# Kernel optimization log

Hardware: AMD Instinct MI355X
Metric: run time of the kernel (lower is better)

The kernel has to match this reference:

```python
import jax, jax.numpy as jnp
import numpy as np


def _roi_crop_resize(fm, proposals, S):
    # fm: [1, H, W, C] channels-last; proposals: [N, 4] (x1, y1, x2, y2) pixel coords.
    # Faithful to: round box coords, clamp to [0, W-1]/[0, H-1], crop fm[:, y1:y2, x1:x2],
    # bilinear tf.image.resize (half-pixel centers) to [S, S]. Implemented as one fused
    # gather-based bilinear sample over all boxes (no data-dependent shapes).
    f = fm[0]  # [H, W, C]
    H, W, _ = f.shape
    b = jnp.round(proposals)
    x1 = jnp.maximum(b[:, 0], 0.0)
    y1 = jnp.maximum(b[:, 1], 0.0)
    x2 = jnp.minimum(b[:, 2], float(W - 1))
    y2 = jnp.minimum(b[:, 3], float(H - 1))
    h = y2 - y1  # crop height per box [N]
    w = x2 - x1  # crop width  per box [N]
    # tf.image.resize bilinear: src = (dst + 0.5) * (in/out) - 0.5, clamped into crop.
    t = (jnp.arange(S, dtype=f.dtype) + 0.5) / S  # [S]
    sy = jnp.clip(t[None, :] * h[:, None] - 0.5, 0.0, jnp.maximum(h[:, None] - 1.0, 0.0)) + y1[:, None]  # [N,S]
    sx = jnp.clip(t[None, :] * w[:, None] - 0.5, 0.0, jnp.maximum(w[:, None] - 1.0, 0.0)) + x1[:, None]  # [N,S]
    y0 = jnp.floor(sy)
    x0 = jnp.floor(sx)
    y0i = y0.astype(jnp.int32)
    x0i = x0.astype(jnp.int32)
    y1i = jnp.minimum(y0i + 1, H - 1)
    x1i = jnp.minimum(x0i + 1, W - 1)
    # Gather 4 bilinear corners: [N, S, S, C]
    v00 = f[y0i[:, :, None], x0i[:, None, :]]
    v01 = f[y0i[:, :, None], x1i[:, None, :]]
    v10 = f[y1i[:, :, None], x0i[:, None, :]]
    v11 = f[y1i[:, :, None], x1i[:, None, :]]
    wy = (sy - y0)[:, :, None, None]  # [N,S,1,1]
    wx = (sx - x0)[:, None, :, None]  # [N,1,S,1]
    top = v00 * (1.0 - wx) + v01 * wx
    bot = v10 * (1.0 - wx) + v11 * wx
    return top * (1.0 - wy) + bot * wy  # [N, S, S, C]


def setup_inputs() -> dict:
    key = jax.random.key(0)
    k1, k2, k3 = jax.random.split(key, 3)
    feature_map = jax.random.normal(k1, (1, 256, 256, 256), dtype=jnp.float32)
    # Valid boxes: centers in-image, half-sizes in [8, 64] so crops are non-degenerate.
    ctr = jax.random.uniform(k2, (1024, 2), minval=16.0, maxval=240.0)
    half = jax.random.uniform(k3, (1024, 2), minval=8.0, maxval=64.0)
    proposals = jnp.stack(
        [ctr[:, 0] - half[:, 0], ctr[:, 1] - half[:, 1],
         ctr[:, 0] + half[:, 0], ctr[:, 1] + half[:, 1]], axis=1
    ).astype(jnp.float32)
    return {"feature_map": feature_map, "proposals": proposals, "roi_size": 7}


def reference(feature_map, proposals, roi_size):
    return _roi_crop_resize(feature_map, proposals, int(roi_size))
```

## Files before the change

kernel.cpp:

```cpp
#include <hip/hip_runtime.h>
#include <math.h>

__global__ __launch_bounds__(256) void roi_align_kernel(
    const float* __restrict__ fm,
    const float* __restrict__ props,
    float* __restrict__ out,
    int S, int nprop, int H, int W, int C)
{
    const int wave = (int)((blockIdx.x * blockDim.x + threadIdx.x) >> 6);
    const int lane = threadIdx.x & 63;
    const int total = nprop * S * S;
    if (wave >= total) return;

    const int n  = wave / (S * S);
    const int ij = wave - n * (S * S);
    const int i  = ij / S;
    const int j  = ij - i * S;

    const float4 p = ((const float4*)props)[n];
    const float x1 = fmaxf(rintf(p.x), 0.0f);
    const float y1 = fmaxf(rintf(p.y), 0.0f);
    const float x2 = fminf(rintf(p.z), (float)(W - 1));
    const float y2 = fminf(rintf(p.w), (float)(H - 1));
    const float h  = y2 - y1;
    const float w  = x2 - x1;

    const float ty = ((float)i + 0.5f) / (float)S;
    const float tx = ((float)j + 0.5f) / (float)S;
    const float sy = fminf(fmaxf(ty * h - 0.5f, 0.0f), fmaxf(h - 1.0f, 0.0f)) + y1;
    const float sx = fminf(fmaxf(tx * w - 0.5f, 0.0f), fmaxf(w - 1.0f, 0.0f)) + x1;

    const float y0f = floorf(sy);
    const float x0f = floorf(sx);
    const int y0i = (int)y0f;
    const int x0i = (int)x0f;
    const int y1i = min(y0i + 1, H - 1);
    const int x1i = min(x0i + 1, W - 1);
    const float wy = sy - y0f;
    const float wx = sx - x0f;
    const float owy = 1.0f - wy;
    const float owx = 1.0f - wx;

    const float4* r00 = (const float4*)(fm + ((size_t)y0i * W + x0i) * C);
    const float4* r01 = (const float4*)(fm + ((size_t)y0i * W + x1i) * C);
    const float4* r10 = (const float4*)(fm + ((size_t)y1i * W + x0i) * C);
    const float4* r11 = (const float4*)(fm + ((size_t)y1i * W + x1i) * C);
    float4* o = (float4*)(out + (size_t)wave * C);

    const int nvec = C >> 2;
    for (int v = lane; v < nvec; v += 64) {
        const float4 v00 = r00[v];
        const float4 v01 = r01[v];
        const float4 v10 = r10[v];
        const float4 v11 = r11[v];
        float4 r;
        r.x = (v00.x * owx + v01.x * wx) * owy + (v10.x * owx + v11.x * wx) * wy;
        r.y = (v00.y * owx + v01.y * wx) * owy + (v10.y * owx + v11.y * wx) * wy;
        r.z = (v00.z * owx + v01.z * wx) * owy + (v10.z * owx + v11.z * wx) * wy;
        r.w = (v00.w * owx + v01.w * wx) * owy + (v10.w * owx + v11.w * wx) * wy;
        o[v] = r;
    }
}

extern "C" void kernel_launch(void* const* d_in, const int* in_sizes, int n_in,
                              void* d_out, int out_size, void* d_ws, size_t ws_size,
                              hipStream_t stream)
{
    const float* fm    = (const float*)d_in[0];
    const float* props = (const float*)d_in[1];
    float* out = (float*)d_out;

    const int H = 256, W = 256, C = 256;
    const int nprop = in_sizes[1] / 4;
    int S = 1;
    {
        const long long per = (long long)nprop * C;
        const long long ss = (long long)out_size / per;
        while ((long long)(S + 1) * (S + 1) <= ss) ++S;
    }

    const int total_waves = nprop * S * S;
    const int waves_per_block = 4;
    const int blocks = (total_waves + waves_per_block - 1) / waves_per_block;
    roi_align_kernel<<<blocks, 256, 0, stream>>>(fm, props, out, S, nprop, H, W, C);
}
```

Baseline: 40.52 us.

## Bucket ROIs spatially per XCD and process one ROI per block with prefetch

Adds a preprocessing kernel that sorts proposals by box centre into 64 Morton-ordered spatial buckets. The main kernel then maps block ids so that consecutive ranks on the same XCD handle spatially nearby ROIs, which should improve L2 reuse of feature-map rows. Each block handles one ROI: its four waves loop over the 49 output cells, prefetching the next cell's corner vectors and writing results with nontemporal stores. The cost is an extra single-block launch with shared-memory atomics, plus a specialised path that only handles S=7 and C=256.

```diff
diff --git a/kernel.cpp b/kernel.cpp
--- a/kernel.cpp
+++ b/kernel.cpp
@@ -1,7 +1,121 @@
 #include <hip/hip_runtime.h>
 #include <math.h>
 
-__global__ __launch_bounds__(256) void roi_align_kernel(
+typedef float nfloat4 __attribute__((ext_vector_type(4)));
+
+__global__ __launch_bounds__(256) void bucket_perm(
+    const float4* __restrict__ props, unsigned int* __restrict__ perm, int nprop)
+{
+    __shared__ unsigned int hist[64];
+    __shared__ unsigned int base[64];
+    const int t = threadIdx.x;
+    if (t < 64) hist[t] = 0u;
+    __syncthreads();
+
+    for (int i = t; i < nprop; i += 256) {
+        const float4 p = props[i];
+        const int cx = min(max((int)(0.5f * (p.x + p.z)), 0), 255);
+        const int cy = min(max((int)(0.5f * (p.y + p.w)), 0), 255);
+        const int gx = cx >> 5, gy = cy >> 5;
+        const unsigned int m = (gx & 1) | ((gy & 1) << 1) | ((gx & 2) << 1)
+                             | ((gy & 2) << 2) | ((gx & 4) << 2) | ((gy & 4) << 3);
+        atomicAdd(&hist[m], 1u);
+    }
+    __syncthreads();
+    if (t == 0) {
+        unsigned int s = 0;
+        for (int b = 0; b < 64; ++b) { base[b] = s; s += hist[b]; }
+    }
+    __syncthreads();
+    for (int i = t; i < nprop; i += 256) {
+        const float4 p = props[i];
+        const int cx = min(max((int)(0.5f * (p.x + p.z)), 0), 255);
+        const int cy = min(max((int)(0.5f * (p.y + p.w)), 0), 255);
+        const int gx = cx >> 5, gy = cy >> 5;
+        const unsigned int m = (gx & 1) | ((gy & 1) << 1) | ((gx & 2) << 1)
+                             | ((gy & 2) << 2) | ((gx & 4) << 2) | ((gy & 4) << 3);
+        const unsigned int pos = atomicAdd(&base[m], 1u);
+        perm[pos] = (unsigned int)i;
+    }
+}
+
+template<int S>
+__global__ __launch_bounds__(256) void roi_block(
+    const float* __restrict__ fm,
+    const float4* __restrict__ props,
+    const unsigned int* __restrict__ perm,
+    float* __restrict__ out,
+    int nprop, int H, int W)
+{
+    constexpr int C = 256, SS = S * S;
+    const int nblk = gridDim.x;
+    const int bid = blockIdx.x;
+    const int q = nblk >> 3, r = nblk & 7;
+    const int xcd = bid & 7, pos = bid >> 3;
+    const int rank = (xcd < r ? xcd * (q + 1) : r * (q + 1) + (xcd - r) * q) + pos;
+    if (rank >= nprop) return;
+    const int n = (int)perm[rank];
+
+    const int lane = threadIdx.x & 63;
+    const int wid  = threadIdx.x >> 6;
+
+    const float4 pr = props[n];
+    const float x1 = fmaxf(rintf(pr.x), 0.0f);
+    const float y1 = fmaxf(rintf(pr.y), 0.0f);
+    const float x2 = fminf(rintf(pr.z), (float)(W - 1));
+    const float y2 = fminf(rintf(pr.w), (float)(H - 1));
+    const float h  = y2 - y1;
+    const float w  = x2 - x1;
+    const float hc = fmaxf(h - 1.0f, 0.0f);
+    const float wc = fmaxf(w - 1.0f, 0.0f);
+
+    float* outn = out + (size_t)n * SS * C;
+
+#define ROI_SETUP(ij_, rr_, wxo_, wyo_) {                                        \
+        const int i_ = (ij_) / S, j_ = (ij_) - i_ * S;                           \
+        const float sy_ = fminf(fmaxf((((float)i_ + 0.5f) / (float)S) * h - 0.5f,\
+                                      0.0f), hc) + y1;                           \
+        const float sx_ = fminf(fmaxf((((float)j_ + 0.5f) / (float)S) * w - 0.5f,\
+                                      0.0f), wc) + x1;                           \
+        const float y0f_ = floorf(sy_), x0f_ = floorf(sx_);                      \
+        const int y0i_ = (int)y0f_, x0i_ = (int)x0f_;                            \
+        const int y1i_ = min(y0i_ + 1, H - 1), x1i_ = min(x0i_ + 1, W - 1);      \
+        wyo_ = sy_ - y0f_; wxo_ = sx_ - x0f_;                                    \
+        rr_[0] = (const float4*)(fm + ((size_t)y0i_ * W + x0i_) * C);            \
+        rr_[1] = (const float4*)(fm + ((size_t)y0i_ * W + x1i_) * C);            \
+        rr_[2] = (const float4*)(fm + ((size_t)y1i_ * W + x0i_) * C);            \
+        rr_[3] = (const float4*)(fm + ((size_t)y1i_ * W + x1i_) * C);            \
+    }
+
+    int ij = wid;
+    const float4* ra[4]; float wxa, wya;
+    ROI_SETUP(ij, ra, wxa, wya);
+    float4 va0 = ra[0][lane], va1 = ra[1][lane], va2 = ra[2][lane], va3 = ra[3][lane];
+
+    while (true) {
+        const int ijn = ij + 4;
+        const bool more = (ijn < SS);
+        const float4* rb[4]; float wxb = 0.f, wyb = 0.f;
+        float4 vb0, vb1, vb2, vb3;
+        if (more) {
+            ROI_SETUP(ijn, rb, wxb, wyb);
+            vb0 = rb[0][lane]; vb1 = rb[1][lane]; vb2 = rb[2][lane]; vb3 = rb[3][lane];
+        }
+        const float owx = 1.0f - wxa, owy = 1.0f - wya;
+        nfloat4 res;
+        res.x = (va0.x * owx + va1.x * wxa) * owy + (va2.x * owx + va3.x * wxa) * wya;
+        res.y = (va0.y * owx + va1.y * wxa) * owy + (va2.y * owx + va3.y * wxa) * wya;
+        res.z = (va0.z * owx + va1.z * wxa) * owy + (va2.z * owx + va3.z * wxa) * wya;
+        res.w = (va0.w * owx + va1.w * wxa) * owy + (va2.w * owx + va3.w * wxa) * wya;
+        __builtin_nontemporal_store(res, (nfloat4*)(outn + (size_t)ij * C) + lane);
+        if (!more) break;
+        va0 = vb0; va1 = vb1; va2 = vb2; va3 = vb3;
+        wxa = wxb; wya = wyb; ij = ijn;
+    }
+#undef ROI_SETUP
+}
+
+__global__ __launch_bounds__(256) void roi_align_generic(
     const float* __restrict__ fm,
     const float* __restrict__ props,
     float* __restrict__ out,
@@ -17,18 +131,18 @@
     const int i  = ij / S;
     const int j  = ij - i * S;
 
-    const float4 p = ((const float4*)props)[n];
-    const float x1 = fmaxf(rintf(p.x), 0.0f);
-    const float y1 = fmaxf(rintf(p.y), 0.0f);
-    const float x2 = fminf(rintf(p.z), (float)(W - 1));
-    const float y2 = fminf(rintf(p.w), (float)(H - 1));
+    const float4 pr = ((const float4*)props)[n];
+    const float x1 = fmaxf(rintf(pr.x), 0.0f);
+    const float y1 = fmaxf(rintf(pr.y), 0.0f);
+    const float x2 = fminf(rintf(pr.z), (float)(W - 1));
+    const float y2 = fminf(rintf(pr.w), (float)(H - 1));
     const float h  = y2 - y1;
     const float w  = x2 - x1;
 
-    const float ty = ((float)i + 0.5f) / (float)S;
-    const float tx = ((float)j + 0.5f) / (float)S;
-    const float sy = fminf(fmaxf(ty * h - 0.5f, 0.0f), fmaxf(h - 1.0f, 0.0f)) + y1;
-    const float sx = fminf(fmaxf(tx * w - 0.5f, 0.0f), fmaxf(w - 1.0f, 0.0f)) + x1;
+    const float sy = fminf(fmaxf((((float)i + 0.5f) / (float)S) * h - 0.5f, 0.0f),
+                           fmaxf(h - 1.0f, 0.0f)) + y1;
+    const float sx = fminf(fmaxf((((float)j + 0.5f) / (float)S) * w - 0.5f, 0.0f),
+                           fmaxf(w - 1.0f, 0.0f)) + x1;
 
     const float y0f = floorf(sy);
     const float x0f = floorf(sx);
@@ -36,10 +150,8 @@
     const int x0i = (int)x0f;
     const int y1i = min(y0i + 1, H - 1);
     const int x1i = min(x0i + 1, W - 1);
-    const float wy = sy - y0f;
-    const float wx = sx - x0f;
-    const float owy = 1.0f - wy;
-    const float owx = 1.0f - wx;
+    const float wy = sy - y0f, owy = 1.0f - wy;
+    const float wx = sx - x0f, owx = 1.0f - wx;
 
     const float4* r00 = (const float4*)(fm + ((size_t)y0i * W + x0i) * C);
     const float4* r01 = (const float4*)(fm + ((size_t)y0i * W + x1i) * C);
@@ -79,8 +191,14 @@
         while ((long long)(S + 1) * (S + 1) <= ss) ++S;
     }
 
-    const int total_waves = nprop * S * S;
-    const int waves_per_block = 4;
-    const int blocks = (total_waves + waves_per_block - 1) / waves_per_block;
-    roi_align_kernel<<<blocks, 256, 0, stream>>>(fm, props, out, S, nprop, H, W, C);
-}
+    if (S == 7 && C == 256 && (size_t)nprop * sizeof(unsigned int) <= ws_size) {
+        unsigned int* perm = (unsigned int*)d_ws;
+        bucket_perm<<<1, 256, 0, stream>>>((const float4*)props, perm, nprop);
+        roi_block<7><<<nprop, 256, 0, stream>>>(fm, (const float4*)props, perm,
+                                                out, nprop, H, W);
+    } else {
+        const int total_waves = nprop * S * S;
+        const int blocks = (total_waves + 3) / 4;
+        roi_align_generic<<<blocks, 256, 0, stream>>>(fm, props, out, S, nprop, H, W, C);
+    }
+}
```

Measured after the change: 36.94 us, median of 3. -8.9%, faster.

## Stage feature-map tiles in LDS and bin ROI samples per tile

Applied to the files above, without the earlier changes.

Adds a specialised kernel for S=7, C=256. Each block loads one 17x17-pixel, 64-channel slice of the feature map into LDS using global_load_lds. It then scans all proposals and builds an LDS list of the output samples whose top-left corner falls in its tile. The bilinear interpolation reads the four corners from LDS, and the results are written with nontemporal stores. This aims to replace redundant, scattered global gathers with one streaming pass over the feature map. The cost is reading the whole map, a large LDS footprint that limits occupancy, and a fixed record cap that could drop samples if a tile is very dense.

```diff
diff --git a/kernel.cpp b/kernel.cpp
--- a/kernel.cpp
+++ b/kernel.cpp
@@ -1,7 +1,151 @@
 #include <hip/hip_runtime.h>
 #include <math.h>
 
-__global__ __launch_bounds__(256) void roi_align_kernel(
+typedef float nfloat4 __attribute__((ext_vector_type(4)));
+
+#define TILE   16
+#define TPX    17
+#define NPIX   289
+#define NPIX_PAD 304
+#define CSLICE 64
+#define LREC_CAP 1024
+
+__device__ __forceinline__ void roi_box(const float4 pr, float& x1, float& y1,
+                                        float& w, float& h, float& wc, float& hc) {
+    #pragma clang fp contract(off)
+    x1 = fmaxf(rintf(pr.x), 0.0f);
+    y1 = fmaxf(rintf(pr.y), 0.0f);
+    const float x2 = fminf(rintf(pr.z), 255.0f);
+    const float y2 = fminf(rintf(pr.w), 255.0f);
+    w = x2 - x1; h = y2 - y1;
+    wc = fmaxf(w - 1.0f, 0.0f); hc = fmaxf(h - 1.0f, 0.0f);
+}
+
+__device__ __forceinline__ void roi_sample(float c1, float len, float lenc, int q,
+                                           int* f_out, float* w_out) {
+    #pragma clang fp contract(off)
+    const float tq = ((float)q + 0.5f) / 7.0f;
+    const float s  = fminf(fmaxf(tq * len - 0.5f, 0.0f), lenc) + c1;
+    const float f  = floorf(s);
+    *f_out = (int)f;
+    *w_out = s - f;
+}
+
+__global__ __launch_bounds__(256) void roi_tile_gather(
+    const float* __restrict__ fm,
+    const float4* __restrict__ props,
+    float* __restrict__ out,
+    int nprop)
+{
+    __shared__ float tile[NPIX_PAD * CSLICE];
+    __shared__ unsigned short lrec[LREC_CAP];
+    __shared__ int lcnt;
+
+    const int tid  = threadIdx.x;
+    const int wid  = tid >> 6;
+    const int lane = tid & 63;
+    const int bid  = blockIdx.x;
+    const int t    = bid >> 2;
+    const int cs   = bid & 3;
+    const int Ax   = (t & 15) * TILE;
+    const int Ay   = (t >> 4) * TILE;
+
+    if (tid == 0) lcnt = 0;
+    __syncthreads();
+
+    float4 pp[4]; int pn[4]; int nl = 0;
+    for (int n = tid; n < nprop && nl < 4; n += 256) { pp[nl] = props[n]; pn[nl] = n; ++nl; }
+    __builtin_amdgcn_sched_barrier(0);
+
+    typedef const __attribute__((address_space(1))) unsigned int* gp_t;
+    typedef __attribute__((address_space(3))) unsigned int* lp_t;
+    for (int k = 0; k < 19; ++k) {
+        const int pix0 = k * 16 + (wid << 2);
+        const int p    = pix0 + (lane >> 4);
+        const int ps   = p > 288 ? 288 : p;
+        const int dy   = ps / 17, dx = ps - dy * 17;
+        const int py   = min(Ay + dy, 255);
+        const int px   = min(Ax + dx, 255);
+        const float* src = fm + (size_t)(py * 256 + px) * 256 + cs * CSLICE
+                              + ((lane & 15) << 2);
+        __builtin_amdgcn_global_load_lds((gp_t)src, (lp_t)&tile[pix0 * CSLICE], 16, 0, 0);
+    }
+
+    for (int k = 0; k < nl; ++k) {
+        const int n = pn[k];
+        float x1, y1, w, h, wc, hc;
+        roi_box(pp[k], x1, y1, w, h, wc, hc);
+        if (x1 >= (float)(Ax + TILE) || x1 + wc < (float)Ax) continue;
+        if (y1 >= (float)(Ay + TILE) || y1 + hc < (float)Ay) continue;
+        int mj = 0, mi = 0;
+        #pragma unroll
+        for (int j = 0; j < 7; ++j) {
+            int f; float wdum;
+            roi_sample(x1, w, wc, j, &f, &wdum);
+            if ((unsigned)(f - Ax) < (unsigned)TILE) mj |= 1 << j;
+        }
+        if (!mj) continue;
+        #pragma unroll
+        for (int i = 0; i < 7; ++i) {
+            int f; float wdum;
+            roi_sample(y1, h, hc, i, &f, &wdum);
+            if ((unsigned)(f - Ay) < (unsigned)TILE) mi |= 1 << i;
+        }
+        if (!mi) continue;
+        const int np = __popc((unsigned)mi) * __popc((unsigned)mj);
+        int slot = atomicAdd(&lcnt, np);
+        for (int ii = mi; ii; ii &= ii - 1) {
+            const int i = __ffs(ii) - 1;
+            for (int jj = mj; jj; jj &= jj - 1) {
+                const int j = __ffs(jj) - 1;
+                if (slot < LREC_CAP)
+                    lrec[slot] = (unsigned short)((n << 6) | (i * 7 + j));
+                ++slot;
+            }
+        }
+    }
+
+    __syncthreads();
+
+    const int lc = min(lcnt, LREC_CAP);
+    const int cw = (lane & 15) << 2;
+    for (int base = 0; base < lc; base += 16) {
+        const int idx = base + (wid << 2) + (lane >> 4);
+        if (idx >= lc) break;
+        const int rec = lrec[idx];
+        const int n  = rec >> 6;
+        const int ij = rec & 63;
+        const int i  = ij / 7, j = ij - i * 7;
+
+        float x1, y1, w, h, wc, hc;
+        roi_box(props[n], x1, y1, w, h, wc, hc);
+        int fx, fy; float wx, wy;
+        roi_sample(x1, w, wc, j, &fx, &wx);
+        roi_sample(y1, h, hc, i, &fy, &wy);
+
+        const int lx0 = fx - Ax;
+        const int ly0 = fy - Ay;
+        const int lx1 = min(fx + 1, 255) - Ax;
+        const int ly1 = min(fy + 1, 255) - Ay;
+
+        const nfloat4 v00 = *(const nfloat4*)&tile[(ly0 * TPX + lx0) * CSLICE + cw];
+        const nfloat4 v01 = *(const nfloat4*)&tile[(ly0 * TPX + lx1) * CSLICE + cw];
+        const nfloat4 v10 = *(const nfloat4*)&tile[(ly1 * TPX + lx0) * CSLICE + cw];
+        const nfloat4 v11 = *(const nfloat4*)&tile[(ly1 * TPX + lx1) * CSLICE + cw];
+
+        const float owx = 1.0f - wx, owy = 1.0f - wy;
+        nfloat4 r;
+        r.x = (v00.x * owx + v01.x * wx) * owy + (v10.x * owx + v11.x * wx) * wy;
+        r.y = (v00.y * owx + v01.y * wx) * owy + (v10.y * owx + v11.y * wx) * wy;
+        r.z = (v00.z * owx + v01.z * wx) * owy + (v10.z * owx + v11.z * wx) * wy;
+        r.w = (v00.w * owx + v01.w * wx) * owy + (v10.w * owx + v11.w * wx) * wy;
+
+        float* dst = out + (size_t)(n * 49 + ij) * 256 + cs * CSLICE + cw;
+        __builtin_nontemporal_store(r, (nfloat4*)dst);
+    }
+}
+
+__global__ __launch_bounds__(256) void roi_align_generic(
     const float* __restrict__ fm,
     const float* __restrict__ props,
     float* __restrict__ out,
@@ -17,18 +161,18 @@
     const int i  = ij / S;
     const int j  = ij - i * S;
 
-    const float4 p = ((const float4*)props)[n];
-    const float x1 = fmaxf(rintf(p.x), 0.0f);
-    const float y1 = fmaxf(rintf(p.y), 0.0f);
-    const float x2 = fminf(rintf(p.z), (float)(W - 1));
-    const float y2 = fminf(rintf(p.w), (float)(H - 1));
+    const float4 pr = ((const float4*)props)[n];
+    const float x1 = fmaxf(rintf(pr.x), 0.0f);
+    const float y1 = fmaxf(rintf(pr.y), 0.0f);
+    const float x2 = fminf(rintf(pr.z), (float)(W - 1));
+    const float y2 = fminf(rintf(pr.w), (float)(H - 1));
     const float h  = y2 - y1;
     const float w  = x2 - x1;
 
-    const float ty = ((float)i + 0.5f) / (float)S;
-    const float tx = ((float)j + 0.5f) / (float)S;
-    const float sy = fminf(fmaxf(ty * h - 0.5f, 0.0f), fmaxf(h - 1.0f, 0.0f)) + y1;
-    const float sx = fminf(fmaxf(tx * w - 0.5f, 0.0f), fmaxf(w - 1.0f, 0.0f)) + x1;
+    const float sy = fminf(fmaxf((((float)i + 0.5f) / (float)S) * h - 0.5f, 0.0f),
+                           fmaxf(h - 1.0f, 0.0f)) + y1;
+    const float sx = fminf(fmaxf((((float)j + 0.5f) / (float)S) * w - 0.5f, 0.0f),
+                           fmaxf(w - 1.0f, 0.0f)) + x1;
 
     const float y0f = floorf(sy);
     const float x0f = floorf(sx);
@@ -36,10 +180,8 @@
     const int x0i = (int)x0f;
     const int y1i = min(y0i + 1, H - 1);
     const int x1i = min(x0i + 1, W - 1);
-    const float wy = sy - y0f;
-    const float wx = sx - x0f;
-    const float owy = 1.0f - wy;
-    const float owx = 1.0f - wx;
+    const float wy = sy - y0f, owy = 1.0f - wy;
+    const float wx = sx - x0f, owx = 1.0f - wx;
 
     const float4* r00 = (const float4*)(fm + ((size_t)y0i * W + x0i) * C);
     const float4* r01 = (const float4*)(fm + ((size_t)y0i * W + x1i) * C);
@@ -69,6 +211,7 @@
     const float* fm    = (const float*)d_in[0];
     const float* props = (const float*)d_in[1];
     float* out = (float*)d_out;
+    (void)d_ws; (void)ws_size;
 
     const int H = 256, W = 256, C = 256;
     const int nprop = in_sizes[1] / 4;
@@ -79,8 +222,11 @@
         while ((long long)(S + 1) * (S + 1) <= ss) ++S;
     }
 
-    const int total_waves = nprop * S * S;
-    const int waves_per_block = 4;
-    const int blocks = (total_waves + waves_per_block - 1) / waves_per_block;
-    roi_align_kernel<<<blocks, 256, 0, stream>>>(fm, props, out, S, nprop, H, W, C);
-}
+    if (S == 7 && C == 256 && nprop <= 1024) {
+        roi_tile_gather<<<1024, 256, 0, stream>>>(fm, (const float4*)props, out, nprop);
+    } else {
+        const int total_waves = nprop * S * S;
+        const int blocks = (total_waves + 3) / 4;
+        roi_align_generic<<<blocks, 256, 0, stream>>>(fm, props, out, S, nprop, H, W, C);
+    }
+}
```

New measurement: 45.23 us. 11.6% more time.
